# Kernel optimization log

Hardware: AMD Instinct MI355X
Metric: run time of the kernel (lower is better)

Reference implementation:

```python
import jax, jax.numpy as jnp
import numpy as np

N, E, E_LBL = 50000, 800000, 200000
D_IN, H = 128, 128


def setup_inputs() -> dict:
    key = jax.random.key(0)
    ks = jax.random.split(key, 12)
    s = 0.05
    return {
        "x": jax.random.normal(ks[0], (N, D_IN), jnp.float32),
        "edge_index": jax.random.randint(ks[1], (2, E), 0, N, jnp.int64),
        "edge_label_index": jax.random.randint(ks[2], (2, E_LBL), 0, N, jnp.int64),
        "pre_w": jax.random.normal(ks[3], (D_IN, H), jnp.float32) * s,
        "pre_b": jax.random.normal(ks[4], (H,), jnp.float32) * s,
        "Wx": jax.random.normal(ks[5], (3, 2, H, H), jnp.float32) * s,  # gates z,r,h x cheb orders T0,T1
        "bx": jax.random.normal(ks[6], (3, H), jnp.float32) * s,
        "Wh": jax.random.normal(ks[7], (3, 2, H, H), jnp.float32) * s,
        "bh": jax.random.normal(ks[8], (3, H), jnp.float32) * s,
        "post_w": jax.random.normal(ks[9], (H, 2), jnp.float32) * s,
        "post_b": jax.random.normal(ks[10], (2,), jnp.float32) * s,
    }


def reference(x, edge_index, edge_label_index, pre_w, pre_b, Wx, bx, Wh, bh, post_w, post_b):
    n = x.shape[0]
    src, dst = edge_index[0], edge_index[1]

    # Scaled Chebyshev Laplacian (sym norm, lambda_max=2): L_hat = -D^{-1/2} A D^{-1/2}
    # (diagonal of L_hat is exactly 0, so only off-diagonal edge terms remain).
    deg = jax.ops.segment_sum(jnp.ones_like(src, dtype=x.dtype), src, num_segments=n)
    dinv = jnp.where(deg > 0, jax.lax.rsqrt(jnp.maximum(deg, 1.0)), 0.0)
    w = -(dinv[src] * dinv[dst])  # [E]

    def lap(v):  # L_hat @ v : gather src rows, weight, scatter-add at dst
        return jax.ops.segment_sum(w[:, None] * v[src], dst, num_segments=n)

    def cheb(v, Lv, W2, b):  # ChebConv K=2: T0(v)@W0 + T1(v)@W1 + b
        return v @ W2[0] + Lv @ W2[1] + b

    # pre: Linear(input_dim -> hidden)
    Xh = x @ pre_w + pre_b  # [N, H]
    LX = lap(Xh)

    # GConvGRU single step, H0 = 0
    Hc = jnp.zeros_like(Xh)
    LH = lap(Hc)
    Z = jax.nn.sigmoid(cheb(Xh, LX, Wx[0], bx[0]) + cheb(Hc, LH, Wh[0], bh[0]))
    R = jax.nn.sigmoid(cheb(Xh, LX, Wx[1], bx[1]) + cheb(Hc, LH, Wh[1], bh[1]))
    HR = Hc * R
    LHR = lap(HR)
    Ht = jnp.tanh(cheb(Xh, LX, Wx[2], bx[2]) + cheb(HR, LHR, Wh[2], bh[2]))
    Hc = Z * Hc + (1.0 - Z) * Ht

    h = jax.nn.relu(Hc)
    # link decoder: gather endpoints, hadamard, Linear(H->2), sum over logits
    hprod = h[edge_label_index[0]] * h[edge_label_index[1]]  # [E_lbl, H]
    out = hprod @ post_w + post_b  # [E_lbl, 2]
    return jnp.sum(out, axis=-1)  # [E_lbl]
```

## Files before the change

### kernel.cpp

```cpp
#include <hip/hip_runtime.h>
#include <math.h>


#define RND 2048
#define EPT 8
#define SORT_CAP 1536
#define CAPB 6144

typedef __attribute__((ext_vector_type(4))) float f32x4;
typedef __attribute__((ext_vector_type(8))) short short8;

static __device__ __forceinline__ unsigned short f2b(float f) {
  union { float f; unsigned u; } v; v.f = f;
  unsigned r = (v.u + 0x7fffu + ((v.u >> 16) & 1u)) >> 16;
  return (unsigned short)r;
}
static __device__ __forceinline__ float b2f(unsigned short s) {
  union { unsigned u; float f; } v; v.u = ((unsigned)s) << 16;
  return v.f;
}

__global__ __launch_bounds__(256) void prep_kernel(const float* __restrict__ pre_w, const float* __restrict__ Wx,
                                                   const float* __restrict__ bx, const float* __restrict__ bh,
                                                   const float* __restrict__ post_w, const float* __restrict__ post_b,
                                                   unsigned short* __restrict__ Bt1c, unsigned short* __restrict__ Btc2,
                                                   float* __restrict__ fb2, float* __restrict__ pwsum,
                                                   int* __restrict__ deg, int* __restrict__ binPos, int N) {
  int e = blockIdx.x * 256 + threadIdx.x;
  const int TOT = gridDim.x * 256;
  for (int i = e; i < N; i += TOT) deg[i] = 0;
  if (e < 256) binPos[e] = e * CAPB;
  if (e < 16384) {
    int kc = e >> 12, r = e & 4095, col = r >> 5, kk = r & 31;
    Bt1c[e] = f2b(pre_w[(kc * 32 + kk) * 128 + col]);
  }
  int e2 = e - 16384;
  if (e2 >= 0 && e2 < 65536) {
    int kc = e2 >> 13, r = e2 & 8191, cB = r >> 5, kk = r & 31;
    int k = kc * 32 + kk, half = k >> 7, ki = k & 127;
    int cb = cB >> 7, r7 = cB & 127, nw6 = r7 >> 6, u2 = r7 & 63;
    int g = (u2 >= 32) ? 2 : 0, hcol = cb * 64 + nw6 * 32 + (u2 & 31);
    Btc2[e2] = f2b(Wx[((g * 2 + half) * 128 + ki) * 128 + hcol]);
  }
  int e3 = e - (16384 + 65536);
  if (e3 >= 0 && e3 < 256) {
    int cB = e3;
    int cb = cB >> 7, r7 = cB & 127, nw6 = r7 >> 6, u2 = r7 & 63;
    int g = (u2 >= 32) ? 2 : 0, hcol = cb * 64 + nw6 * 32 + (u2 & 31);
    fb2[cB] = bx[g * 128 + hcol] + bh[g * 128 + hcol];
  }
  int e4 = e - (16384 + 65536 + 256);
  if (e4 >= 0 && e4 < 128) pwsum[e4] = post_w[2 * e4] + post_w[2 * e4 + 1];
  if (e4 == 128) pwsum[128] = post_b[0] + post_b[1];
}

union SMemU {
  struct { unsigned short As[128 * 40]; unsigned short Bs[128 * 40]; } g;
  struct { int hist[256], lofs[256], gbase[256]; } s;
};

__global__ __launch_bounds__(256) void mega1_kernel(const float* __restrict__ x,
                                                    const unsigned short* __restrict__ Bt1c,
                                                    const float* __restrict__ pre_b,
                                                    unsigned short* __restrict__ Xq,
                                                    const int* __restrict__ ei, int* __restrict__ binPos,
                                                    unsigned* __restrict__ bins, int* __restrict__ deg,
                                                    int N, int E, int RB) {
  __shared__ SMemU sm;
  const int t = threadIdx.x;

  if ((int)blockIdx.x < RB) {
    unsigned short* As = sm.g.As;
    unsigned short* Bs = sm.g.Bs;
    const int r0 = blockIdx.x * 128;
    const int w = t >> 6, lane = t & 63;
    const int m = lane & 15, q = lane >> 4;
    const int mw = (w >> 1) * 64, nw = (w & 1) * 64;

    f32x4 acc[4][4];
#pragma unroll
    for (int i = 0; i < 4; ++i)
#pragma unroll
      for (int j = 0; j < 4; ++j) acc[i][j] = {0.f, 0.f, 0.f, 0.f};

    const int arow = t >> 1, aseg = t & 1;
    const bool arow_ok = (r0 + arow) < N;
    const float* asrc0 = &x[(size_t)(r0 + arow) * 128 + aseg * 16];

    float4 cav[4]; short8 cbv0, cbv1;
    {
      if (arow_ok) {
#pragma unroll
        for (int i = 0; i < 4; ++i) cav[i] = *(const float4*)(asrc0 + i * 4);
      } else {
#pragma unroll
        for (int i = 0; i < 4; ++i) cav[i] = make_float4(0.f, 0.f, 0.f, 0.f);
      }
      const char* src = (const char*)Bt1c + t * 32;
      cbv0 = *(const short8*)src;
      cbv1 = *(const short8*)(src + 16);
    }

    for (int kc = 0; kc < 4; ++kc) {
      __syncthreads();
      {
        short8 t0, t1;
#pragma unroll
        for (int i = 0; i < 2; ++i) {
          t0[i * 4 + 0] = (short)f2b(cav[i].x); t0[i * 4 + 1] = (short)f2b(cav[i].y);
          t0[i * 4 + 2] = (short)f2b(cav[i].z); t0[i * 4 + 3] = (short)f2b(cav[i].w);
          t1[i * 4 + 0] = (short)f2b(cav[i + 2].x); t1[i * 4 + 1] = (short)f2b(cav[i + 2].y);
          t1[i * 4 + 2] = (short)f2b(cav[i + 2].z); t1[i * 4 + 3] = (short)f2b(cav[i + 2].w);
        }
        *(short8*)&As[arow * 40 + aseg * 16] = t0;
        *(short8*)&As[arow * 40 + aseg * 16 + 8] = t1;
        int bcol = t >> 1, boff = (t & 1) * 16;
        *(short8*)&Bs[bcol * 40 + boff] = cbv0;
        *(short8*)&Bs[bcol * 40 + boff + 8] = cbv1;
      }
      float4 nav[4]; short8 nbv0, nbv1;
      if (kc < 3) {
        if (arow_ok) {
          const float* src = asrc0 + (kc + 1) * 32;
#pragma unroll
          for (int i = 0; i < 4; ++i) nav[i] = *(const float4*)(src + i * 4);
        } else {
#pragma unroll
          for (int i = 0; i < 4; ++i) nav[i] = make_float4(0.f, 0.f, 0.f, 0.f);
        }
        const char* src = (const char*)Bt1c + (size_t)(kc + 1) * 8192 + t * 32;
        nbv0 = *(const short8*)src;
        nbv1 = *(const short8*)(src + 16);
      }
      __syncthreads();
      short8 af[4], bf[4];
#pragma unroll
      for (int i = 0; i < 4; ++i) af[i] = *(const short8*)&As[(mw + i * 16 + m) * 40 + q * 8];
#pragma unroll
      for (int j = 0; j < 4; ++j) bf[j] = *(const short8*)&Bs[(nw + j * 16 + m) * 40 + q * 8];
#pragma unroll
      for (int i = 0; i < 4; ++i)
#pragma unroll
        for (int j = 0; j < 4; ++j)
          acc[i][j] = __builtin_amdgcn_mfma_f32_16x16x32_bf16(af[i], bf[j], acc[i][j], 0, 0, 0);
      if (kc < 3) {
#pragma unroll
        for (int i = 0; i < 4; ++i) cav[i] = nav[i];
        cbv0 = nbv0; cbv1 = nbv1;
      }
    }

#pragma unroll
    for (int i = 0; i < 4; ++i) {
      int rb2 = r0 + mw + i * 16 + q * 4;
#pragma unroll
      for (int j = 0; j < 4; ++j) {
        int col = nw + j * 16 + m;
        float bias = pre_b[col];
#pragma unroll
        for (int r = 0; r < 4; ++r) {
          int row = rb2 + r;
          if (row < N) Xq[(size_t)row * 128 + col] = f2b(acc[i][j][r] + bias);
        }
      }
    }
    return;
  }

  int* hist = sm.s.hist;
  int* lofs = sm.s.lofs;
  int* gbase = sm.s.gbase;
  const int sbid = (int)blockIdx.x - RB;
  const int snum = (int)gridDim.x - RB;
  for (long long base = (long long)sbid * RND; base < E; base += (long long)snum * RND) {
    int cnt = (int)(((long long)E - base < RND) ? (E - base) : RND);
    if (t < 256) { hist[t] = 0; lofs[t] = 0; }
    __syncthreads();
    unsigned my_e[EPT]; int my_b[EPT];
#pragma unroll
    for (int u = 0; u < EPT; ++u) {
      int i = u * 256 + t;
      my_b[u] = -1;
      if (i < cnt) {
        int idx = (int)base + i;
        int s = ei[idx], d = ei[E + idx];
        atomicAdd(&deg[s], 1);
        my_b[u] = d >> 8;
        my_e[u] = (unsigned)s | ((unsigned)(d & 255) << 16);
        atomicAdd(&hist[my_b[u]], 1);
      }
    }
    __syncthreads();
    if (t < 256 && hist[t] > 0) gbase[t] = atomicAdd(&binPos[t], hist[t]);
    __syncthreads();
#pragma unroll
    for (int u = 0; u < EPT; ++u) {
      if (my_b[u] >= 0) {
        int b = my_b[u];
        int p = atomicAdd(&lofs[b], 1);
        int pos = gbase[b] + p;
        if (pos < (b + 1) * CAPB) bins[pos] = my_e[u];
      }
    }
    __syncthreads();
  }
}

__global__ __launch_bounds__(512) void lap_bin_kernel(const unsigned short* __restrict__ Xq,
                                                      unsigned short* __restrict__ LXc,
                                                      const unsigned* __restrict__ bins,
                                                      const int* __restrict__ binPos,
                                                      const int* __restrict__ deg, int N) {
  __shared__ unsigned short sortS[SORT_CAP];
  __shared__ float sortW[SORT_CAP];
  __shared__ int hist[64], start[64], scanbuf[64], off[64];
  const int t = threadIdx.x;
  const int bin = blockIdx.x >> 2, qt = blockIdx.x & 3;
  const int lo = bin * CAPB;
  int T = binPos[bin] - lo;
  if (T > CAPB) T = CAPB;
  const unsigned* __restrict__ ebase = &bins[lo];
  if (t < 64) hist[t] = 0;
  __syncthreads();
  for (int i = t; i < T; i += 512) {
    unsigned e = ebase[i];
    int dl = (e >> 16) & 255;
    if ((dl >> 6) == qt) atomicAdd(&hist[dl & 63], 1);
  }
  __syncthreads();
  if (t < 64) scanbuf[t] = hist[t];
  __syncthreads();
  for (int d = 1; d < 64; d <<= 1) {
    int v = (t < 64 && t >= d) ? scanbuf[t - d] : 0;
    __syncthreads();
    if (t < 64) scanbuf[t] += v;
    __syncthreads();
  }
  if (t < 64) { int s0 = scanbuf[t] - hist[t]; start[t] = s0; off[t] = s0; }
  __syncthreads();
  for (int i = t; i < T; i += 512) {
    unsigned e = ebase[i];
    int dl = (e >> 16) & 255;
    if ((dl >> 6) == qt) {
      int s = (int)(e & 0xFFFFu);
      int p = atomicAdd(&off[dl & 63], 1);
      if (p < SORT_CAP) {
        int dg = deg[s];
        sortS[p] = (unsigned short)s;
        sortW[p] = dg > 0 ? rsqrtf((float)dg) : 0.0f;
      }
    }
  }
  __syncthreads();
  const int wv = t >> 6, lane = t & 63;
  for (int n = wv; n < 64; n += 8) {
    int node = bin * 256 + qt * 64 + n;
    if (node >= N) break;
    int st = start[n], cnum = hist[n];
    float ax = 0.f, ay = 0.f;
    for (int j = 0; j < cnum; j += 8) {
      unsigned v[8]; float ws[8];
#pragma unroll
      for (int u = 0; u < 8; ++u) {
        int idx = j + u;
        int s = 0; float w = 0.f;
        if (idx < cnum) { s = sortS[st + idx]; w = sortW[st + idx]; }
        ws[u] = w;
        v[u] = *(const unsigned*)((const char*)Xq + (size_t)s * 256 + lane * 4);
      }
#pragma unroll
      for (int u = 0; u < 8; ++u) {
        union { unsigned u32; float f; } fl, fh;
        fl.u32 = v[u] << 16; fh.u32 = v[u] & 0xffff0000u;
        ax += ws[u] * fl.f;
        ay += ws[u] * fh.f;
      }
    }
    int dgn = deg[node];
    float wd = dgn > 0 ? -rsqrtf((float)dgn) : 0.0f;
    unsigned o = (unsigned)f2b(ax * wd) | ((unsigned)f2b(ay * wd) << 16);
    *(unsigned*)((char*)LXc + (size_t)node * 256 + lane * 4) = o;
  }
}

__global__ __launch_bounds__(256) void gemm2_mfma(const unsigned short* __restrict__ Xq,
                                                  const unsigned short* __restrict__ LXc,
                                                  const unsigned short* __restrict__ Btc2,
                                                  const float* __restrict__ fb2,
                                                  unsigned short* __restrict__ hb, int N) {
  __shared__ unsigned short As[128 * 40];
  __shared__ unsigned short Bs[128 * 40];
  const int t = threadIdx.x;
  const int rb = blockIdx.x >> 1, cb = blockIdx.x & 1;
  const int r0 = rb * 128;
  const int w = t >> 6, lane = t & 63;
  const int m = lane & 15, q = lane >> 4;
  const int mw = (w >> 1) * 64, nw = (w & 1) * 64;

  f32x4 acc[4][4];
#pragma unroll
  for (int i = 0; i < 4; ++i)
#pragma unroll
    for (int j = 0; j < 4; ++j) acc[i][j] = {0.f, 0.f, 0.f, 0.f};

  const int arow = t >> 1;
  const int aoff = (t & 1) * 32;
  const char* aXq = (const char*)Xq + (size_t)(r0 + arow) * 256 + aoff;
  const char* aLX = (const char*)LXc + (size_t)(r0 + arow) * 256 + aoff;
  const char* bsrc0 = (const char*)Btc2 + (size_t)cb * 8192 + t * 32;

  short8 cav0, cav1, cbv0, cbv1;
  cav0 = *(const short8*)aXq;
  cav1 = *(const short8*)(aXq + 16);
  cbv0 = *(const short8*)bsrc0;
  cbv1 = *(const short8*)(bsrc0 + 16);

  for (int kc = 0; kc < 8; ++kc) {
    __syncthreads();
    *(short8*)&As[arow * 40 + (aoff >> 1)] = cav0;
    *(short8*)&As[arow * 40 + (aoff >> 1) + 8] = cav1;
    {
      int bcol = t >> 1, boff = (t & 1) * 16;
      *(short8*)&Bs[bcol * 40 + boff] = cbv0;
      *(short8*)&Bs[bcol * 40 + boff + 8] = cbv1;
    }
    short8 nav0, nav1, nbv0, nbv1;
    if (kc < 7) {
      int kn = kc + 1;
      const char* asrc = (kn < 4) ? (aXq + kn * 64) : (aLX + (kn - 4) * 64);
      nav0 = *(const short8*)asrc;
      nav1 = *(const short8*)(asrc + 16);
      const char* bsrc = bsrc0 + (size_t)kn * 16384;
      nbv0 = *(const short8*)bsrc;
      nbv1 = *(const short8*)(bsrc + 16);
    }
    __syncthreads();
    short8 af[4], bf[4];
#pragma unroll
    for (int i = 0; i < 4; ++i) af[i] = *(const short8*)&As[(mw + i * 16 + m) * 40 + q * 8];
#pragma unroll
    for (int j = 0; j < 4; ++j) bf[j] = *(const short8*)&Bs[(nw + j * 16 + m) * 40 + q * 8];
#pragma unroll
    for (int i = 0; i < 4; ++i)
#pragma unroll
      for (int j = 0; j < 4; ++j)
        acc[i][j] = __builtin_amdgcn_mfma_f32_16x16x32_bf16(af[i], bf[j], acc[i][j], 0, 0, 0);
    if (kc < 7) { cav0 = nav0; cav1 = nav1; cbv0 = nbv0; cbv1 = nbv1; }
  }

#pragma unroll
  for (int i = 0; i < 4; ++i) {
    int rbase = r0 + mw + i * 16 + q * 4;
#pragma unroll
    for (int jz = 0; jz < 2; ++jz) {
      int cBz = cb * 128 + nw + jz * 16 + m;
      int hc = cb * 64 + (nw >> 1) + jz * 16 + m;
      float bz = fb2[cBz], bt = fb2[cBz + 32];
#pragma unroll
      for (int r = 0; r < 4; ++r) {
        int row = rbase + r;
        if (row < N) {
          float zp = acc[i][jz][r] + bz;
          float tp = acc[i][jz + 2][r] + bt;
          float zs = 1.0f / (1.0f + __expf(-zp));
          float th = tanhf(tp);
          hb[(size_t)row * 128 + hc] = f2b(fmaxf((1.0f - zs) * th, 0.0f));
        }
      }
    }
  }
}

__global__ __launch_bounds__(256) void decoder_kernel(const unsigned short* __restrict__ hb,
                                                      const int* __restrict__ eli,
                                                      const float* __restrict__ pwsum, float* __restrict__ out, int M) {
  int t = threadIdx.x;
  int i = blockIdx.x * 16 + (t >> 4);
  int l = t & 15;
  if (i >= M) return;
  int a = eli[i], b = eli[M + i];
  int k = l * 8;
  short8 va = *(const short8*)&hb[(size_t)a * 128 + k];
  short8 vb = *(const short8*)&hb[(size_t)b * 128 + k];
  const float4* pwp = (const float4*)&pwsum[k];
  float4 p0 = pwp[0], p1 = pwp[1];
  float s = 0.0f;
  s += b2f((unsigned short)va[0]) * b2f((unsigned short)vb[0]) * p0.x;
  s += b2f((unsigned short)va[1]) * b2f((unsigned short)vb[1]) * p0.y;
  s += b2f((unsigned short)va[2]) * b2f((unsigned short)vb[2]) * p0.z;
  s += b2f((unsigned short)va[3]) * b2f((unsigned short)vb[3]) * p0.w;
  s += b2f((unsigned short)va[4]) * b2f((unsigned short)vb[4]) * p1.x;
  s += b2f((unsigned short)va[5]) * b2f((unsigned short)vb[5]) * p1.y;
  s += b2f((unsigned short)va[6]) * b2f((unsigned short)vb[6]) * p1.z;
  s += b2f((unsigned short)va[7]) * b2f((unsigned short)vb[7]) * p1.w;
#pragma unroll
  for (int off = 8; off; off >>= 1) s += __shfl_xor(s, off);
  if (l == 0) out[i] = s + pwsum[128];
}

extern "C" void kernel_launch(void* const* d_in, const int* in_sizes, int n_in,
                              void* d_out, int out_size, void* d_ws, size_t ws_size,
                              hipStream_t stream) {
  const float* x      = (const float*)d_in[0];
  const int*   ei     = (const int*)d_in[1];
  const int*   eli    = (const int*)d_in[2];
  const float* pre_w  = (const float*)d_in[3];
  const float* pre_b  = (const float*)d_in[4];
  const float* Wx     = (const float*)d_in[5];
  const float* bx     = (const float*)d_in[6];
  const float* bh     = (const float*)d_in[8];
  const float* post_w = (const float*)d_in[9];
  const float* post_b = (const float*)d_in[10];
  float* out = (float*)d_out;

  const int N = in_sizes[0] / 128;
  const int E = in_sizes[1] / 2;
  const int M = in_sizes[2] / 2;
  const int RB = (N + 127) / 128;
  const int NBIN = (N + 255) / 256;
  const int SCAT = (E + RND - 1) / RND;

  char* W = (char*)d_ws;
  size_t o = 0;
  int* deg = (int*)(W + o);       o += (size_t)N * 4;
  int* binPos = (int*)(W + o);    o += 1024;
  o = (o + 255) & ~(size_t)255;
  unsigned* bins = (unsigned*)(W + o); o += (size_t)NBIN * CAPB * 4;
  o = (o + 255) & ~(size_t)255;
  unsigned short* Xq = (unsigned short*)(W + o);  o += (size_t)RB * 128 * 256;
  unsigned short* LXc = (unsigned short*)(W + o); o += (size_t)RB * 128 * 256;
  unsigned short* hb = (unsigned short*)(W + o);  o += (size_t)N * 256;
  unsigned short* Bt1c = (unsigned short*)(W + o); o += 32768;
  unsigned short* Btc2 = (unsigned short*)(W + o); o += 131072;
  float* fb2 = (float*)(W + o);  o += 1024;
  float* pwsum = (float*)(W + o); o += 768;

  prep_kernel<<<322, 256, 0, stream>>>(pre_w, Wx, bx, bh, post_w, post_b, Bt1c, Btc2, fb2, pwsum,
                                       deg, binPos, N);
  mega1_kernel<<<RB + SCAT, 256, 0, stream>>>(x, Bt1c, pre_b, Xq, ei, binPos, bins, deg, N, E, RB);
  lap_bin_kernel<<<NBIN * 4, 512, 0, stream>>>(Xq, LXc, bins, binPos, deg, N);
  gemm2_mfma<<<RB * 2, 256, 0, stream>>>(Xq, LXc, Btc2, fb2, hb, N);
  decoder_kernel<<<(M + 15) / 16, 256, 0, stream>>>(hb, eli, pwsum, out, M);
}
```

Baseline: 215.6 us.

## Replace global atomic bin cursors with per-block fixed-capacity edge buckets

```diff
diff --git a/kernel.cpp b/kernel.cpp
--- a/kernel.cpp
+++ b/kernel.cpp
@@ -4,8 +4,9 @@
 
 #define RND 2048
 #define EPT 8
+#define CAP2 32
 #define SORT_CAP 1536
-#define CAPB 6144
+#define MAXSC 768
 
 typedef __attribute__((ext_vector_type(4))) float f32x4;
 typedef __attribute__((ext_vector_type(8))) short short8;
@@ -25,11 +26,10 @@
                                                    const float* __restrict__ post_w, const float* __restrict__ post_b,
                                                    unsigned short* __restrict__ Bt1c, unsigned short* __restrict__ Btc2,
                                                    float* __restrict__ fb2, float* __restrict__ pwsum,
-                                                   int* __restrict__ deg, int* __restrict__ binPos, int N) {
+                                                   int* __restrict__ deg, int N) {
   int e = blockIdx.x * 256 + threadIdx.x;
   const int TOT = gridDim.x * 256;
   for (int i = e; i < N; i += TOT) deg[i] = 0;
-  if (e < 256) binPos[e] = e * CAPB;
   if (e < 16384) {
     int kc = e >> 12, r = e & 4095, col = r >> 5, kk = r & 31;
     Bt1c[e] = f2b(pre_w[(kc * 32 + kk) * 128 + col]);
@@ -56,16 +56,17 @@
 
 union SMemU {
   struct { unsigned short As[128 * 40]; unsigned short Bs[128 * 40]; } g;
-  struct { int hist[256], lofs[256], gbase[256]; } s;
+  struct { int cur[256]; } s;
 };
 
 __global__ __launch_bounds__(256) void mega1_kernel(const float* __restrict__ x,
                                                     const unsigned short* __restrict__ Bt1c,
                                                     const float* __restrict__ pre_b,
                                                     unsigned short* __restrict__ Xq,
-                                                    const int* __restrict__ ei, int* __restrict__ binPos,
-                                                    unsigned* __restrict__ bins, int* __restrict__ deg,
-                                                    int N, int E, int RB) {
+                                                    const int* __restrict__ ei,
+                                                    unsigned* __restrict__ bins2, int* __restrict__ cnt2,
+                                                    int* __restrict__ deg,
+                                                    int N, int E, int RB, int SC) {
   __shared__ SMemU sm;
   const int t = threadIdx.x;
 
@@ -167,65 +168,54 @@
     return;
   }
 
-  int* hist = sm.s.hist;
-  int* lofs = sm.s.lofs;
-  int* gbase = sm.s.gbase;
+  int* cur = sm.s.cur;
   const int sbid = (int)blockIdx.x - RB;
-  const int snum = (int)gridDim.x - RB;
-  for (long long base = (long long)sbid * RND; base < E; base += (long long)snum * RND) {
-    int cnt = (int)(((long long)E - base < RND) ? (E - base) : RND);
-    if (t < 256) { hist[t] = 0; lofs[t] = 0; }
-    __syncthreads();
-    unsigned my_e[EPT]; int my_b[EPT];
-#pragma unroll
-    for (int u = 0; u < EPT; ++u) {
-      int i = u * 256 + t;
-      my_b[u] = -1;
-      if (i < cnt) {
-        int idx = (int)base + i;
-        int s = ei[idx], d = ei[E + idx];
-        atomicAdd(&deg[s], 1);
-        my_b[u] = d >> 8;
-        my_e[u] = (unsigned)s | ((unsigned)(d & 255) << 16);
-        atomicAdd(&hist[my_b[u]], 1);
-      }
-    }
-    __syncthreads();
-    if (t < 256 && hist[t] > 0) gbase[t] = atomicAdd(&binPos[t], hist[t]);
-    __syncthreads();
-#pragma unroll
-    for (int u = 0; u < EPT; ++u) {
-      if (my_b[u] >= 0) {
-        int b = my_b[u];
-        int p = atomicAdd(&lofs[b], 1);
-        int pos = gbase[b] + p;
-        if (pos < (b + 1) * CAPB) bins[pos] = my_e[u];
-      }
-    }
-    __syncthreads();
+  const long long base = (long long)sbid * RND;
+  const int cnt = (int)((((long long)E - base) < RND) ? ((long long)E - base) : RND);
+  if (t < 256) cur[t] = 0;
+  __syncthreads();
+#pragma unroll
+  for (int u = 0; u < EPT; ++u) {
+    int i = u * 256 + t;
+    if (i < cnt) {
+      int idx = (int)base + i;
+      int s = ei[idx], d = ei[E + idx];
+      atomicAdd(&deg[s], 1);
+      int b = d >> 8;
+      unsigned e = (unsigned)s | ((unsigned)(d & 255) << 16);
+      int p = atomicAdd(&cur[b], 1);
+      if (p < CAP2) bins2[((size_t)b * SC + sbid) * CAP2 + p] = e;
+    }
+  }
+  __syncthreads();
+  if (t < 256) {
+    int c = cur[t];
+    cnt2[(size_t)t * SC + sbid] = (c < CAP2) ? c : CAP2;
   }
 }
 
 __global__ __launch_bounds__(512) void lap_bin_kernel(const unsigned short* __restrict__ Xq,
                                                       unsigned short* __restrict__ LXc,
-                                                      const unsigned* __restrict__ bins,
-                                                      const int* __restrict__ binPos,
-                                                      const int* __restrict__ deg, int N) {
+                                                      const unsigned* __restrict__ bins2,
+                                                      const int* __restrict__ cnt2,
+                                                      const int* __restrict__ deg, int N, int SC) {
   __shared__ unsigned short sortS[SORT_CAP];
   __shared__ float sortW[SORT_CAP];
   __shared__ int hist[64], start[64], scanbuf[64], off[64];
+  __shared__ int cnts[MAXSC];
   const int t = threadIdx.x;
   const int bin = blockIdx.x >> 2, qt = blockIdx.x & 3;
-  const int lo = bin * CAPB;
-  int T = binPos[bin] - lo;
-  if (T > CAPB) T = CAPB;
-  const unsigned* __restrict__ ebase = &bins[lo];
   if (t < 64) hist[t] = 0;
-  __syncthreads();
-  for (int i = t; i < T; i += 512) {
-    unsigned e = ebase[i];
-    int dl = (e >> 16) & 255;
-    if ((dl >> 6) == qt) atomicAdd(&hist[dl & 63], 1);
+  for (int i = t; i < SC; i += 512) cnts[i] = cnt2[(size_t)bin * SC + i];
+  __syncthreads();
+  const int TOTSLOT = SC * CAP2;
+  const unsigned* __restrict__ rbase = &bins2[(size_t)bin * SC * CAP2];
+  for (int idx = t; idx < TOTSLOT; idx += 512) {
+    if ((idx & (CAP2 - 1)) < cnts[idx / CAP2]) {
+      unsigned e = rbase[idx];
+      int dl = (e >> 16) & 255;
+      if ((dl >> 6) == qt) atomicAdd(&hist[dl & 63], 1);
+    }
   }
   __syncthreads();
   if (t < 64) scanbuf[t] = hist[t];
@@ -238,16 +228,18 @@
   }
   if (t < 64) { int s0 = scanbuf[t] - hist[t]; start[t] = s0; off[t] = s0; }
   __syncthreads();
-  for (int i = t; i < T; i += 512) {
-    unsigned e = ebase[i];
-    int dl = (e >> 16) & 255;
-    if ((dl >> 6) == qt) {
-      int s = (int)(e & 0xFFFFu);
-      int p = atomicAdd(&off[dl & 63], 1);
-      if (p < SORT_CAP) {
-        int dg = deg[s];
-        sortS[p] = (unsigned short)s;
-        sortW[p] = dg > 0 ? rsqrtf((float)dg) : 0.0f;
+  for (int idx = t; idx < TOTSLOT; idx += 512) {
+    if ((idx & (CAP2 - 1)) < cnts[idx / CAP2]) {
+      unsigned e = rbase[idx];
+      int dl = (e >> 16) & 255;
+      if ((dl >> 6) == qt) {
+        int s = (int)(e & 0xFFFFu);
+        int p = atomicAdd(&off[dl & 63], 1);
+        if (p < SORT_CAP) {
+          int dg = deg[s];
+          sortS[p] = (unsigned short)s;
+          sortW[p] = dg > 0 ? rsqrtf((float)dg) : 0.0f;
+        }
       }
     }
   }
@@ -418,14 +410,14 @@
   const int M = in_sizes[2] / 2;
   const int RB = (N + 127) / 128;
   const int NBIN = (N + 255) / 256;
-  const int SCAT = (E + RND - 1) / RND;
+  const int SC = (E + RND - 1) / RND;
 
   char* W = (char*)d_ws;
   size_t o = 0;
   int* deg = (int*)(W + o);       o += (size_t)N * 4;
-  int* binPos = (int*)(W + o);    o += 1024;
   o = (o + 255) & ~(size_t)255;
-  unsigned* bins = (unsigned*)(W + o); o += (size_t)NBIN * CAPB * 4;
+  unsigned* bins2 = (unsigned*)(W + o); o += (size_t)256 * SC * CAP2 * 4;
+  int* cnt2 = (int*)(W + o);      o += (size_t)256 * SC * 4;
   o = (o + 255) & ~(size_t)255;
   unsigned short* Xq = (unsigned short*)(W + o);  o += (size_t)RB * 128 * 256;
   unsigned short* LXc = (unsigned short*)(W + o); o += (size_t)RB * 128 * 256;
@@ -436,9 +428,9 @@
   float* pwsum = (float*)(W + o); o += 768;
 
   prep_kernel<<<322, 256, 0, stream>>>(pre_w, Wx, bx, bh, post_w, post_b, Bt1c, Btc2, fb2, pwsum,
-                                       deg, binPos, N);
-  mega1_kernel<<<RB + SCAT, 256, 0, stream>>>(x, Bt1c, pre_b, Xq, ei, binPos, bins, deg, N, E, RB);
-  lap_bin_kernel<<<NBIN * 4, 512, 0, stream>>>(Xq, LXc, bins, binPos, deg, N);
+                                       deg, N);
+  mega1_kernel<<<RB + SC, 256, 0, stream>>>(x, Bt1c, pre_b, Xq, ei, bins2, cnt2, deg, N, E, RB, SC);
+  lap_bin_kernel<<<NBIN * 4, 512, 0, stream>>>(Xq, LXc, bins2, cnt2, deg, N, SC);
   gemm2_mfma<<<RB * 2, 256, 0, stream>>>(Xq, LXc, Btc2, fb2, hb, N);
   decoder_kernel<<<(M + 15) / 16, 256, 0, stream>>>(hb, eli, pwsum, out, M);
 }
```

After: 229.6 us. +6.5%, slower.
